# Optimization experiments

Hardware: AMD Instinct MI355X
Metric: run time of the kernel (lower is better)

## Reference

```python
import jax, jax.numpy as jnp
import numpy as np

SEQ, BATCH, HIDDEN = 2048, 2, 1024
NUM_HEADS, HEAD_DIM = 16, 64
LN_EPS = 1e-6
NEG_INF = -1e10


def setup_inputs() -> dict:
    key = jax.random.key(0)
    k1, k2, k3 = jax.random.split(key, 3)
    inputs_q = jax.random.normal(k1, (SEQ, BATCH, HIDDEN), dtype=jnp.float32)
    ln_scale = jnp.ones((HIDDEN,), dtype=jnp.float32)
    ln_bias = jnp.zeros((HIDDEN,), dtype=jnp.float32)
    # fused QKV kernel: (hidden, 3, num_heads*head_dim), fan_in variance scaling
    qkv_kernel = jax.random.normal(k2, (HIDDEN, 3, NUM_HEADS * HEAD_DIM), dtype=jnp.float32) / np.sqrt(HIDDEN).astype(np.float32)
    out_kernel = jax.random.normal(k3, (NUM_HEADS * HEAD_DIM, HIDDEN), dtype=jnp.float32) / np.sqrt(NUM_HEADS * HEAD_DIM).astype(np.float32)
    return {"inputs_q": inputs_q, "ln_scale": ln_scale, "ln_bias": ln_bias,
            "qkv_kernel": qkv_kernel, "out_kernel": out_kernel}


def reference(inputs_q, ln_scale, ln_bias, qkv_kernel, out_kernel):
    s, b, h = inputs_q.shape
    # --- LayerNorm (fused with QKV projection in the original module) ---
    mu = jnp.mean(inputs_q, axis=-1, keepdims=True)
    var = jnp.mean(jnp.square(inputs_q - mu), axis=-1, keepdims=True)
    ln_out = (inputs_q - mu) * jax.lax.rsqrt(var + LN_EPS) * ln_scale + ln_bias
    # --- fused QKV projection: (s,b,h) @ (h,3,nh*hd) -> (s,b,3,nh*hd) ---
    qkv = jnp.einsum('sbh,htk->stbk', ln_out, qkv_kernel)  # (s,3,b,nh*hd)
    q = qkv[:, 0].reshape(s, b, NUM_HEADS, HEAD_DIM)  # (s,b,nh,hd)
    k = qkv[:, 1].reshape(s, b, NUM_HEADS, HEAD_DIM)
    v = qkv[:, 2].reshape(s, b, NUM_HEADS, HEAD_DIM)
    # --- core attention (transpose_batch_sequence=True layout) ---
    scale = 1.0 / np.sqrt(HEAD_DIM).astype(np.float32)  # scale_attn_logits=True
    logits = jnp.einsum('qbhd,kbhd->bhqk', q, k) * scale
    causal = jnp.tril(jnp.ones((s, s), dtype=bool))  # attn_mask_type='causal'
    logits = jnp.where(causal[None, None], logits, jnp.asarray(NEG_INF, logits.dtype))
    attn = jax.nn.softmax(logits, axis=-1)
    ctx = jnp.einsum('bhqk,kbhd->qbhd', attn, v).reshape(s, b, NUM_HEADS * HEAD_DIM)
    # --- output projection ---
    return jnp.einsum('sbk,kh->sbh', ctx, out_kernel)
```

## Files before the change

kernel.cpp:

```cpp
#include <hip/hip_runtime.h>

typedef unsigned short u16;
typedef unsigned int u32;
typedef __attribute__((ext_vector_type(8))) short short8;
typedef __attribute__((ext_vector_type(4))) float f32x4;

#define AS1C(p) ((const __attribute__((address_space(1))) void*)(p))
#define AS3(p)  ((__attribute__((address_space(3))) void*)(p))

constexpr int SEQ = 2048, BATCH = 2, HIDDEN = 1024, NH = 16, HD = 64;
constexpr int MROWS = SEQ * BATCH;
constexpr int QKV_N = 3 * NH * HD;
#define Q_SCALE 0.18033688011112042f

__device__ __forceinline__ float bf2f(u16 u) {
  union { u32 i; float f; } v; v.i = (u32)u << 16; return v.f;
}
__device__ __forceinline__ u16 f2bf(float f) {
  union { float f; u32 i; } v; v.f = f;
  u32 r = v.i + 0x7fffu + ((v.i >> 16) & 1u);
  return (u16)(r >> 16);
}
__device__ __forceinline__ u32 cvt_pk_bf16(float lo, float hi) {
  u32 r;
  asm("v_cvt_pk_bf16_f32 %0, %1, %2" : "=v"(r) : "v"(lo), "v"(hi));
  return r;
}
__device__ __forceinline__ bool is_f32(const unsigned* probe) { return probe[0] == 0x3F800000u; }

__global__ __launch_bounds__(256) void transpose2_k(const void* __restrict__ wqkv,
                                                    u16* __restrict__ qkvT,
                                                    const void* __restrict__ wout,
                                                    u16* __restrict__ outT,
                                                    const unsigned* __restrict__ probe) {
  __shared__ alignas(16) u16 t[32][33];
  const bool fm = is_f32(probe);
  const int bx = blockIdx.x;
  const void* in;
  u16* out;
  int C, c0;
  if (bx < 96) { in = wqkv; out = qkvT; C = QKV_N; c0 = bx * 32; }
  else         { in = wout; out = outT; C = HIDDEN; c0 = (bx - 96) * 32; }
  const int r0 = blockIdx.y * 32;
  int tx = threadIdx.x & 31, ty = threadIdx.x >> 5;
  if (fm) {
    const float* fin = (const float*)in;
#pragma unroll
    for (int i = 0; i < 32; i += 8) t[ty + i][tx] = f2bf(fin[(size_t)(r0 + ty + i) * C + c0 + tx]);
  } else {
    const u16* uin = (const u16*)in;
#pragma unroll
    for (int i = 0; i < 32; i += 8) t[ty + i][tx] = uin[(size_t)(r0 + ty + i) * C + c0 + tx];
  }
  __syncthreads();
#pragma unroll
  for (int i = 0; i < 32; i += 8) out[(size_t)(c0 + ty + i) * HIDDEN + r0 + tx] = t[tx][ty + i];
}

__global__ __launch_bounds__(256) void ln_k(const void* __restrict__ xv, const void* __restrict__ gv,
                                            const void* __restrict__ bv, u16* __restrict__ y,
                                            const unsigned* __restrict__ probe) {
  const bool fm = is_f32(probe);
  int row = blockIdx.x, t = threadIdx.x;
  float f0, f1, f2, f3, g0, g1, g2, g3, b0, b1, b2, b3;
  if (fm) {
    float4 v = *(const float4*)((const float*)xv + (size_t)row * HIDDEN + t * 4);
    f0 = v.x; f1 = v.y; f2 = v.z; f3 = v.w;
    float4 gg = *(const float4*)((const float*)gv + t * 4);
    g0 = gg.x; g1 = gg.y; g2 = gg.z; g3 = gg.w;
    float4 bb = *(const float4*)((const float*)bv + t * 4);
    b0 = bb.x; b1 = bb.y; b2 = bb.z; b3 = bb.w;
  } else {
    ushort4 v = *(const ushort4*)((const u16*)xv + (size_t)row * HIDDEN + t * 4);
    f0 = bf2f(v.x); f1 = bf2f(v.y); f2 = bf2f(v.z); f3 = bf2f(v.w);
    ushort4 gg = *(const ushort4*)((const u16*)gv + t * 4);
    g0 = bf2f(gg.x); g1 = bf2f(gg.y); g2 = bf2f(gg.z); g3 = bf2f(gg.w);
    ushort4 bb = *(const ushort4*)((const u16*)bv + t * 4);
    b0 = bf2f(bb.x); b1 = bf2f(bb.y); b2 = bf2f(bb.z); b3 = bf2f(bb.w);
  }
  float s = f0 + f1 + f2 + f3;
  float s2 = f0 * f0 + f1 * f1 + f2 * f2 + f3 * f3;
#pragma unroll
  for (int off = 1; off < 64; off <<= 1) { s += __shfl_xor(s, off); s2 += __shfl_xor(s2, off); }
  __shared__ float ps[4], ps2[4];
  int w = t >> 6, lane = t & 63;
  if (lane == 0) { ps[w] = s; ps2[w] = s2; }
  __syncthreads();
  s = ps[0] + ps[1] + ps[2] + ps[3];
  s2 = ps2[0] + ps2[1] + ps2[2] + ps2[3];
  float mu = s * (1.0f / HIDDEN);
  float rstd = rsqrtf(s2 * (1.0f / HIDDEN) - mu * mu + 1e-6f);
  ushort4 o;
  o.x = f2bf((f0 - mu) * rstd * g0 + b0);
  o.y = f2bf((f1 - mu) * rstd * g1 + b1);
  o.z = f2bf((f2 - mu) * rstd * g2 + b2);
  o.w = f2bf((f3 - mu) * rstd * g3 + b3);
  *(ushort4*)(y + (size_t)row * HIDDEN + t * 4) = o;
}

template <int EPI>
__global__ __launch_bounds__(256) void gemm_k(const u16* __restrict__ A, const u16* __restrict__ Bt,
                                              void* __restrict__ o0, u16* __restrict__ o1,
                                              u16* __restrict__ o2, int M, int N, int K,
                                              const unsigned* __restrict__ probe) {
  __shared__ alignas(16) u16 As[2][128 * 32];
  __shared__ alignas(16) u16 Bs[2][128 * 32];
  const int bm = blockIdx.x, bn = blockIdx.y;
  const int tid = threadIdx.x, w = tid >> 6, lane = tid & 63;
  const int wr = w >> 1, wc = w & 1, lr = lane & 15, lk = lane >> 4;
  f32x4 acc[4][4] = {};

  const int srow_lo = lane >> 2;
  const int sslot = lane & 3;
  const int csw = ((lk ^ ((lr >> 1) & 3)) * 8);
  const int nk = K >> 5;

  int srowA[2], srcA[2];
#pragma unroll
  for (int j = 0; j < 2; j++) {
    const int issue = w * 2 + j;
    srowA[j] = issue * 16 + srow_lo;
    srcA[j] = ((sslot ^ ((srowA[j] >> 1) & 3)) * 8);
  }

#define STAGE(kt, bufi)                                                                     \
  {                                                                                         \
    const int k0s = (kt) * 32;                                                              \
    _Pragma("unroll")                                                                       \
    for (int j = 0; j < 2; j++) {                                                           \
      const int issue = w * 2 + j;                                                          \
      __builtin_amdgcn_global_load_lds(                                                     \
          AS1C(A + (size_t)(bm * 128 + srowA[j]) * K + k0s + srcA[j]),                      \
          AS3(As[bufi] + issue * 512 + lane * 8), 16, 0, 0);                                \
      __builtin_amdgcn_global_load_lds(                                                     \
          AS1C(Bt + (size_t)(bn * 128 + srowA[j]) * K + k0s + srcA[j]),                     \
          AS3(Bs[bufi] + issue * 512 + lane * 8), 16, 0, 0);                                \
    }                                                                                       \
  }

  STAGE(0, 0);
  __syncthreads();

  int buf = 0;
  for (int kt = 0; kt < nk; ++kt) {
    if (kt + 1 < nk) STAGE(kt + 1, buf ^ 1);
    short8 a[4], b[4];
#pragma unroll
    for (int i = 0; i < 4; i++) {
      a[i] = *(const short8*)(As[buf] + (wr * 64 + i * 16 + lr) * 32 + csw);
      b[i] = *(const short8*)(Bs[buf] + (wc * 64 + i * 16 + lr) * 32 + csw);
    }
#pragma unroll
    for (int mi = 0; mi < 4; mi++)
#pragma unroll
      for (int ni = 0; ni < 4; ni++)
        acc[mi][ni] = __builtin_amdgcn_mfma_f32_16x16x32_bf16(a[mi], b[ni], acc[mi][ni], 0, 0, 0);
    __syncthreads();
    buf ^= 1;
  }
#undef STAGE

  const int r0 = bm * 128 + wr * 64, c0 = bn * 128 + wc * 64;
  if constexpr (EPI == 0) {
    const bool fm = is_f32(probe);
#pragma unroll
    for (int mi = 0; mi < 4; mi++)
#pragma unroll
      for (int ni = 0; ni < 4; ni++) {
        int col = c0 + ni * 16 + lr;
#pragma unroll
        for (int j = 0; j < 4; j++) {
          int row = r0 + mi * 16 + lk * 4 + j;
          if (fm) ((float*)o0)[(size_t)row * N + col] = acc[mi][ni][j];
          else    ((u16*)o0)[(size_t)row * N + col] = f2bf(acc[mi][ni][j]);
        }
      }
  } else {
#pragma unroll
    for (int mi = 0; mi < 4; mi++)
#pragma unroll
      for (int ni = 0; ni < 4; ni++) {
        int n = c0 + ni * 16 + lr;
        int t = n >> 10, rem = n & 1023, h = rem >> 6, d = rem & 63;
#pragma unroll
        for (int j = 0; j < 4; j++) {
          int r = r0 + mi * 16 + lk * 4 + j;
          int s = r >> 1, bb = r & 1;
          size_t bh = (size_t)(bb * NH + h);
          if (t == 0)      ((u16*)o0)[(bh * SEQ + s) * HD + d] = f2bf(acc[mi][ni][j] * Q_SCALE);
          else if (t == 1) o1[(bh * SEQ + s) * HD + d] = f2bf(acc[mi][ni][j]);
          else             o2[(bh * HD + d) * SEQ + s] = f2bf(acc[mi][ni][j]);
        }
      }
  }
}

__global__ __launch_bounds__(256, 4) void attn_k(const u16* __restrict__ Q, const u16* __restrict__ Kb,
                                                 const u16* __restrict__ VT, u16* __restrict__ ctx) {
  const int flat = blockIdx.x;
  const int xu = flat & 7, idx = flat >> 3;
  const int g = idx >> 2, j = idx & 3;
  const int bh = xu * 4 + j;
  int qt;
  if (j == 0)      qt = g;
  else if (j == 1) qt = 31 - g;
  else if (j == 2) qt = (g + 16) & 31;
  else             qt = (15 - g) & 31;
  const int tid = threadIdx.x;
  const int w = tid >> 6, lane = tid & 63;
  const int lr = lane & 15, lk = lane >> 4;
  const size_t base = (size_t)bh * SEQ * HD;
  const int b = bh >> 4, h = bh & 15;

  __shared__ alignas(16) u16 Ks[2][4096];
  __shared__ alignas(16) u16 Vs[2][4096];
  __shared__ alignas(16) u16 P[4][16 * 64];
  u16* Pw = &P[w][0];
  u32* Pw32 = (u32*)Pw;

  const int st_r = lane >> 3;
  const int st_c = 8 * ((lane & 7) ^ st_r);
  const int swz = (lr & 7) << 3;
  const int psw = (lr & 7) << 1;

  const int qr0 = qt * 64 + w * 16;
  const int qrow = qr0 + lr;
  const int klast = qt;

  short8 aq[2];
#pragma unroll
  for (int kk = 0; kk < 2; kk++)
    aq[kk] = *(const short8*)(Q + base + (size_t)qrow * HD + kk * 32 + lk * 8);

  f32x4 o[4] = {};
  float l = 0.0f;

#pragma unroll
  for (int j2 = 0; j2 < 2; j2++) {
    const int c = j2 * 4 + w;
    const int r = c * 8 + st_r;
    __builtin_amdgcn_global_load_lds(AS1C(Kb + base + (size_t)r * HD + st_c),
                                     AS3(Ks[0] + c * 512), 16, 0, 0);
    __builtin_amdgcn_global_load_lds(AS1C(VT + base + (size_t)r * SEQ + st_c),
                                     AS3(Vs[0] + c * 512), 16, 0, 0);
  }
  __syncthreads();

  for (int kt = 0; kt <= klast; kt++) {
    const int k0 = kt * 64;
    const int buf = kt & 1;
    if (kt < klast) {
      const int kn = k0 + 64;
#pragma unroll
      for (int j2 = 0; j2 < 2; j2++) {
        const int c = j2 * 4 + w;
        const int r = c * 8 + st_r;
        __builtin_amdgcn_global_load_lds(AS1C(Kb + base + (size_t)(kn + r) * HD + st_c),
                                         AS3(Ks[buf ^ 1] + c * 512), 16, 0, 0);
        __builtin_amdgcn_global_load_lds(AS1C(VT + base + (size_t)r * SEQ + kn + st_c),
                                         AS3(Vs[buf ^ 1] + c * 512), 16, 0, 0);
      }
    }
    short8 bk[4][2], bv[4][2];
#pragma unroll
    for (int ni = 0; ni < 4; ni++) {
      const int row = ni * 16 + lr;
#pragma unroll
      for (int kk = 0; kk < 2; kk++)
        bk[ni][kk] = *(const short8*)(Ks[buf] + row * 64 + ((kk * 32 + lk * 8) ^ swz));
#pragma unroll
      for (int ks = 0; ks < 2; ks++)
        bv[ni][ks] = *(const short8*)(Vs[buf] + row * 64 + ((ks * 32 + lk * 8) ^ swz));
    }
    f32x4 s[4] = {};
#pragma unroll
    for (int ni = 0; ni < 4; ni++)
#pragma unroll
      for (int kk = 0; kk < 2; kk++)
        s[ni] = __builtin_amdgcn_mfma_f32_16x16x32_bf16(bk[ni][kk], aq[kk], s[ni], 0, 0, 0);
    if (kt == klast) {
#pragma unroll
      for (int ni = 0; ni < 4; ni++)
#pragma unroll
        for (int jj = 0; jj < 4; jj++)
          if (k0 + ni * 16 + lk * 4 + jj > qrow) s[ni][jj] = -1e30f;
    }
#pragma unroll
    for (int ni = 0; ni < 4; ni++) {
#pragma unroll
      for (int jj = 0; jj < 4; jj++) s[ni][jj] = exp2f(s[ni][jj]);
      l += (s[ni][0] + s[ni][1]) + (s[ni][2] + s[ni][3]);
    }
#pragma unroll
    for (int ni = 0; ni < 4; ni++) {
      uint2 pk;
      pk.x = cvt_pk_bf16(s[ni][0], s[ni][1]);
      pk.y = cvt_pk_bf16(s[ni][2], s[ni][3]);
      *(uint2*)(Pw32 + lr * 32 + 2 * ((4 * ni + lk) ^ psw)) = pk;
    }
    short8 pa[2];
#pragma unroll
    for (int kk = 0; kk < 2; kk++)
      pa[kk] = *(const short8*)(Pw + lr * 64 + 4 * (((kk << 3) + (lk << 1)) ^ psw));
#pragma unroll
    for (int ni = 0; ni < 4; ni++)
#pragma unroll
      for (int kk = 0; kk < 2; kk++)
        o[ni] = __builtin_amdgcn_mfma_f32_16x16x32_bf16(pa[kk], bv[ni][kk], o[ni], 0, 0, 0);
    __syncthreads();
  }
  float lf = l;
  lf += __shfl_xor(lf, 16);
  lf += __shfl_xor(lf, 32);
  float linv0 = 1.0f / __shfl(lf, lk * 4 + 0);
  float linv1 = 1.0f / __shfl(lf, lk * 4 + 1);
  float linv2 = 1.0f / __shfl(lf, lk * 4 + 2);
  float linv3 = 1.0f / __shfl(lf, lk * 4 + 3);
#pragma unroll
  for (int ni = 0; ni < 4; ni++) {
    int col = h * HD + ni * 16 + lr;
    ctx[(size_t)((qr0 + lk * 4 + 0) * BATCH + b) * (NH * HD) + col] = f2bf(o[ni][0] * linv0);
    ctx[(size_t)((qr0 + lk * 4 + 1) * BATCH + b) * (NH * HD) + col] = f2bf(o[ni][1] * linv1);
    ctx[(size_t)((qr0 + lk * 4 + 2) * BATCH + b) * (NH * HD) + col] = f2bf(o[ni][2] * linv2);
    ctx[(size_t)((qr0 + lk * 4 + 3) * BATCH + b) * (NH * HD) + col] = f2bf(o[ni][3] * linv3);
  }
}

extern "C" void kernel_launch(void* const* d_in, const int* in_sizes, int n_in,
                              void* d_out, int out_size, void* d_ws, size_t ws_size,
                              hipStream_t stream) {
  const void* x    = d_in[0];
  const void* g    = d_in[1];
  const void* bta  = d_in[2];
  const void* wqkv = d_in[3];
  const void* wout = d_in[4];
  const unsigned* probe = (const unsigned*)d_in[1];

  char* ws = (char*)d_ws;
  u16* ln   = (u16*)(ws);
  u16* q    = (u16*)(ws + 8388608);
  u16* k    = (u16*)(ws + 16777216);
  u16* vT   = (u16*)(ws + 25165824);
  u16* qkvT = (u16*)(ws + 33554432);
  u16* outT = (u16*)(ws + 33554432 + 6291456);
  u16* ctx  = ln;

  transpose2_k<<<dim3(128, 32), 256, 0, stream>>>(wqkv, qkvT, wout, outT, probe);
  ln_k<<<MROWS, 256, 0, stream>>>(x, g, bta, ln, probe);
  gemm_k<1><<<dim3(MROWS / 128, QKV_N / 128), 256, 0, stream>>>(ln, qkvT, q, k, vT,
                                                                MROWS, QKV_N, HIDDEN, probe);
  attn_k<<<dim3(1024), 256, 0, stream>>>(q, k, vT, ctx);
  gemm_k<0><<<dim3(MROWS / 128, HIDDEN / 128), 256, 0, stream>>>(ctx, outT, d_out, nullptr,
                                                                 nullptr, MROWS, HIDDEN,
                                                                 HIDDEN, probe);
}
```

Before: 119.6 us.

## Merge LayerNorm and weight transposes into one launch; reorder attention tiles heaviest-first

Combines the weight transpose/convert kernel and the LayerNorm kernel into a single pre_k launch that dispatches on block index, removing one kernel launch and the gap between the two. Separately, the attention grid mapping drops the balanced query-tile permutation and schedules causal query tiles from heaviest (last) to lightest, relying on the hardware scheduler to fill gaps. The simpler ordering may change load balance and L2 locality across heads.

```diff
diff --git a/kernel.cpp b/kernel.cpp
--- a/kernel.cpp
+++ b/kernel.cpp
@@ -28,74 +28,71 @@
 }
 __device__ __forceinline__ bool is_f32(const unsigned* probe) { return probe[0] == 0x3F800000u; }
 
-__global__ __launch_bounds__(256) void transpose2_k(const void* __restrict__ wqkv,
-                                                    u16* __restrict__ qkvT,
-                                                    const void* __restrict__ wout,
-                                                    u16* __restrict__ outT,
-                                                    const unsigned* __restrict__ probe) {
-  __shared__ alignas(16) u16 t[32][33];
+__global__ __launch_bounds__(256) void pre_k(const void* __restrict__ xv, const void* __restrict__ gv,
+                                             const void* __restrict__ bv, u16* __restrict__ y,
+                                             const void* __restrict__ wqkv, u16* __restrict__ qkvT,
+                                             const void* __restrict__ wout, u16* __restrict__ outT,
+                                             const unsigned* __restrict__ probe) {
   const bool fm = is_f32(probe);
-  const int bx = blockIdx.x;
-  const void* in;
-  u16* out;
-  int C, c0;
-  if (bx < 96) { in = wqkv; out = qkvT; C = QKV_N; c0 = bx * 32; }
-  else         { in = wout; out = outT; C = HIDDEN; c0 = (bx - 96) * 32; }
-  const int r0 = blockIdx.y * 32;
-  int tx = threadIdx.x & 31, ty = threadIdx.x >> 5;
-  if (fm) {
-    const float* fin = (const float*)in;
-#pragma unroll
-    for (int i = 0; i < 32; i += 8) t[ty + i][tx] = f2bf(fin[(size_t)(r0 + ty + i) * C + c0 + tx]);
+  const int bid = blockIdx.x;
+  if (bid < MROWS) {
+    const int row = bid, t = threadIdx.x;
+    float f0, f1, f2, f3, g0, g1, g2, g3, b0, b1, b2, b3;
+    if (fm) {
+      float4 v = *(const float4*)((const float*)xv + (size_t)row * HIDDEN + t * 4);
+      f0 = v.x; f1 = v.y; f2 = v.z; f3 = v.w;
+      float4 gg = *(const float4*)((const float*)gv + t * 4);
+      g0 = gg.x; g1 = gg.y; g2 = gg.z; g3 = gg.w;
+      float4 bb = *(const float4*)((const float*)bv + t * 4);
+      b0 = bb.x; b1 = bb.y; b2 = bb.z; b3 = bb.w;
+    } else {
+      ushort4 v = *(const ushort4*)((const u16*)xv + (size_t)row * HIDDEN + t * 4);
+      f0 = bf2f(v.x); f1 = bf2f(v.y); f2 = bf2f(v.z); f3 = bf2f(v.w);
+      ushort4 gg = *(const ushort4*)((const u16*)gv + t * 4);
+      g0 = bf2f(gg.x); g1 = bf2f(gg.y); g2 = bf2f(gg.z); g3 = bf2f(gg.w);
+      ushort4 bb = *(const ushort4*)((const u16*)bv + t * 4);
+      b0 = bf2f(bb.x); b1 = bf2f(bb.y); b2 = bf2f(bb.z); b3 = bf2f(bb.w);
+    }
+    float s = f0 + f1 + f2 + f3;
+    float s2 = f0 * f0 + f1 * f1 + f2 * f2 + f3 * f3;
+#pragma unroll
+    for (int off = 1; off < 64; off <<= 1) { s += __shfl_xor(s, off); s2 += __shfl_xor(s2, off); }
+    __shared__ float ps[4], ps2[4];
+    int w = t >> 6, lane = t & 63;
+    if (lane == 0) { ps[w] = s; ps2[w] = s2; }
+    __syncthreads();
+    s = ps[0] + ps[1] + ps[2] + ps[3];
+    s2 = ps2[0] + ps2[1] + ps2[2] + ps2[3];
+    float mu = s * (1.0f / HIDDEN);
+    float rstd = rsqrtf(s2 * (1.0f / HIDDEN) - mu * mu + 1e-6f);
+    ushort4 o;
+    o.x = f2bf((f0 - mu) * rstd * g0 + b0);
+    o.y = f2bf((f1 - mu) * rstd * g1 + b1);
+    o.z = f2bf((f2 - mu) * rstd * g2 + b2);
+    o.w = f2bf((f3 - mu) * rstd * g3 + b3);
+    *(ushort4*)(y + (size_t)row * HIDDEN + t * 4) = o;
   } else {
-    const u16* uin = (const u16*)in;
-#pragma unroll
-    for (int i = 0; i < 32; i += 8) t[ty + i][tx] = uin[(size_t)(r0 + ty + i) * C + c0 + tx];
-  }
-  __syncthreads();
-#pragma unroll
-  for (int i = 0; i < 32; i += 8) out[(size_t)(c0 + ty + i) * HIDDEN + r0 + tx] = t[tx][ty + i];
-}
-
-__global__ __launch_bounds__(256) void ln_k(const void* __restrict__ xv, const void* __restrict__ gv,
-                                            const void* __restrict__ bv, u16* __restrict__ y,
-                                            const unsigned* __restrict__ probe) {
-  const bool fm = is_f32(probe);
-  int row = blockIdx.x, t = threadIdx.x;
-  float f0, f1, f2, f3, g0, g1, g2, g3, b0, b1, b2, b3;
-  if (fm) {
-    float4 v = *(const float4*)((const float*)xv + (size_t)row * HIDDEN + t * 4);
-    f0 = v.x; f1 = v.y; f2 = v.z; f3 = v.w;
-    float4 gg = *(const float4*)((const float*)gv + t * 4);
-    g0 = gg.x; g1 = gg.y; g2 = gg.z; g3 = gg.w;
-    float4 bb = *(const float4*)((const float*)bv + t * 4);
-    b0 = bb.x; b1 = bb.y; b2 = bb.z; b3 = bb.w;
-  } else {
-    ushort4 v = *(const ushort4*)((const u16*)xv + (size_t)row * HIDDEN + t * 4);
-    f0 = bf2f(v.x); f1 = bf2f(v.y); f2 = bf2f(v.z); f3 = bf2f(v.w);
-    ushort4 gg = *(const ushort4*)((const u16*)gv + t * 4);
-    g0 = bf2f(gg.x); g1 = bf2f(gg.y); g2 = bf2f(gg.z); g3 = bf2f(gg.w);
-    ushort4 bb = *(const ushort4*)((const u16*)bv + t * 4);
-    b0 = bf2f(bb.x); b1 = bf2f(bb.y); b2 = bf2f(bb.z); b3 = bf2f(bb.w);
-  }
-  float s = f0 + f1 + f2 + f3;
-  float s2 = f0 * f0 + f1 * f1 + f2 * f2 + f3 * f3;
-#pragma unroll
-  for (int off = 1; off < 64; off <<= 1) { s += __shfl_xor(s, off); s2 += __shfl_xor(s2, off); }
-  __shared__ float ps[4], ps2[4];
-  int w = t >> 6, lane = t & 63;
-  if (lane == 0) { ps[w] = s; ps2[w] = s2; }
-  __syncthreads();
-  s = ps[0] + ps[1] + ps[2] + ps[3];
-  s2 = ps2[0] + ps2[1] + ps2[2] + ps2[3];
-  float mu = s * (1.0f / HIDDEN);
-  float rstd = rsqrtf(s2 * (1.0f / HIDDEN) - mu * mu + 1e-6f);
-  ushort4 o;
-  o.x = f2bf((f0 - mu) * rstd * g0 + b0);
-  o.y = f2bf((f1 - mu) * rstd * g1 + b1);
-  o.z = f2bf((f2 - mu) * rstd * g2 + b2);
-  o.w = f2bf((f3 - mu) * rstd * g3 + b3);
-  *(ushort4*)(y + (size_t)row * HIDDEN + t * 4) = o;
+    __shared__ alignas(16) u16 t[32][33];
+    const int tb = bid - MROWS;
+    const void* in;
+    u16* out;
+    int C, c0, r0;
+    if (tb < 3072) { in = wqkv; out = qkvT; C = QKV_N; c0 = (tb % 96) * 32; r0 = (tb / 96) * 32; }
+    else { const int t2 = tb - 3072; in = wout; out = outT; C = HIDDEN; c0 = (t2 & 31) * 32; r0 = (t2 >> 5) * 32; }
+    int tx = threadIdx.x & 31, ty = threadIdx.x >> 5;
+    if (fm) {
+      const float* fin = (const float*)in;
+#pragma unroll
+      for (int i = 0; i < 32; i += 8) t[ty + i][tx] = f2bf(fin[(size_t)(r0 + ty + i) * C + c0 + tx]);
+    } else {
+      const u16* uin = (const u16*)in;
+#pragma unroll
+      for (int i = 0; i < 32; i += 8) t[ty + i][tx] = uin[(size_t)(r0 + ty + i) * C + c0 + tx];
+    }
+    __syncthreads();
+#pragma unroll
+    for (int i = 0; i < 32; i += 8) out[(size_t)(c0 + ty + i) * HIDDEN + r0 + tx] = t[tx][ty + i];
+  }
 }
 
 template <int EPI>
@@ -199,13 +196,8 @@
                                                  const u16* __restrict__ VT, u16* __restrict__ ctx) {
   const int flat = blockIdx.x;
   const int xu = flat & 7, idx = flat >> 3;
-  const int g = idx >> 2, j = idx & 3;
-  const int bh = xu * 4 + j;
-  int qt;
-  if (j == 0)      qt = g;
-  else if (j == 1) qt = 31 - g;
-  else if (j == 2) qt = (g + 16) & 31;
-  else             qt = (15 - g) & 31;
+  const int bh = xu * 4 + (idx & 3);
+  const int qt = 31 - (idx >> 2);
   const int tid = threadIdx.x;
   const int w = tid >> 6, lane = tid & 63;
   const int lr = lane & 15, lk = lane >> 4;
@@ -345,8 +337,7 @@
   u16* outT = (u16*)(ws + 33554432 + 6291456);
   u16* ctx  = ln;
 
-  transpose2_k<<<dim3(128, 32), 256, 0, stream>>>(wqkv, qkvT, wout, outT, probe);
-  ln_k<<<MROWS, 256, 0, stream>>>(x, g, bta, ln, probe);
+  pre_k<<<dim3(MROWS + 3072 + 1024), 256, 0, stream>>>(x, g, bta, ln, wqkv, qkvT, wout, outT, probe);
   gemm_k<1><<<dim3(MROWS / 128, QKV_N / 128), 256, 0, stream>>>(ln, qkvT, q, k, vT,
                                                                 MROWS, QKV_N, HIDDEN, probe);
   attn_k<<<dim3(1024), 256, 0, stream>>>(q, k, vT, ctx);
```

Result: faster. 110.6 us (-7.6%).
